# Kernel tuning notes

Measured on AMD Instinct MI355X. Metric: run time of the kernel, lower is better.

The kernel has to match this reference:

```python
import jax, jax.numpy as jnp
import numpy as np

B, L, D, H, E, K = 1, 512, 512, 512, 32, 2

def setup_inputs() -> dict:
    key = jax.random.key(0)
    ks = jax.random.split(key, 6)
    x = jax.random.normal(ks[0], (B, L, D), dtype=jnp.float32)
    router_scale = 1.0 + 0.02 * jax.random.normal(ks[1], (D,), dtype=jnp.float32)
    router_logits_w = 0.02 * jax.random.normal(ks[2], (D, E), dtype=jnp.float32)
    gating_einsum = 0.02 * jax.random.normal(ks[3], (E, 2, H, D), dtype=jnp.float32)
    linear_w = 0.02 * jax.random.normal(ks[4], (E, H, D), dtype=jnp.float32)
    per_expert_scale = 1.0 + 0.02 * jax.random.normal(ks[5], (E,), dtype=jnp.float32)
    return {"x": x, "router_scale": router_scale, "router_logits_w": router_logits_w,
            "gating_einsum": gating_einsum, "linear_w": linear_w,
            "per_expert_scale": per_expert_scale}

def reference(x, router_scale, router_logits_w, gating_einsum, linear_w, per_expert_scale):
    d = x.shape[-1]
    n_experts = router_logits_w.shape[-1]
    # RMSNorm without scale (fp32)
    x32 = x.astype(jnp.float32)
    var = jnp.mean(jnp.square(x32), axis=-1, keepdims=True)
    router_input = x32 * jax.lax.rsqrt(var + 1e-6)
    root_size = jax.lax.rsqrt(jnp.asarray(d, dtype=router_input.dtype))
    router_input = router_input * root_size * router_scale.astype(router_input.dtype)
    logits = jnp.dot(router_input, router_logits_w).astype(jnp.float32)  # [B,L,E]
    probs = jax.nn.softmax(logits, axis=-1)
    _, top_k_indices = jax.lax.top_k(logits, K)  # [B,L,K]
    indicator = jax.nn.one_hot(top_k_indices, n_experts, dtype=probs.dtype).sum(axis=-2)
    gate_weights = indicator * probs
    renorm = jnp.sum(gate_weights, axis=-1, keepdims=True)
    renorm = jnp.where(renorm > 0.0, renorm, 1.0)
    weights = probs / renorm
    top_k_weights = jnp.take_along_axis(weights, top_k_indices, axis=-1)  # [B,L,K]
    output = jnp.zeros_like(x)
    for ki in range(K):  # small fixed k; faithful to source's per-slot gather
        expert_idx = top_k_indices[:, :, ki]          # [B,L] int32
        expert_w = top_k_weights[:, :, ki]            # [B,L]
        gate_params = gating_einsum[expert_idx]       # [B,L,2,H,D] -- the big gather
        lin_params = linear_w[expert_idx]             # [B,L,H,D]
        escale = per_expert_scale[expert_idx]         # [B,L]
        gate_0 = jnp.einsum('bld,blhd->blh', x, gate_params[:, :, 0])
        gate_1 = jnp.einsum('bld,blhd->blh', x, gate_params[:, :, 1])
        activated = jax.nn.gelu(gate_0) * gate_1
        expert_out = jnp.einsum('blh,blhd->bld', activated, lin_params)
        output = output + expert_out * (escale * expert_w)[..., None]
    return output
```

## Files before the change

### kernel.cpp

```cpp
#include <hip/hip_runtime.h>
#include <hip/hip_bf16.h>
#include <math.h>

#define LTOK 512
#define DDIM 512
#define NEXP 32
#define HDIM 512

typedef __attribute__((ext_vector_type(8))) short short8;
typedef __attribute__((ext_vector_type(4))) float floatx4;

__device__ __forceinline__ unsigned bpack(float a, float b) {
    unsigned ua = __float_as_uint(a), ub = __float_as_uint(b);
    ua += 0x7FFFu + ((ua >> 16) & 1u);
    ub += 0x7FFFu + ((ub >> 16) & 1u);
    return (ua >> 16) | (ub & 0xFFFF0000u);
}


__global__ __launch_bounds__(64) void router_kernel(
    const float* __restrict__ x, const float* __restrict__ rs,
    const float* __restrict__ Wr, const float* __restrict__ pes,
    int* __restrict__ cnt, int* __restrict__ alist, float* __restrict__ slist,
    short* __restrict__ xb)
{
    const int t = blockIdx.x;
    const int lane = threadIdx.x;

    float xv[8];
    float ss = 0.f;
#pragma unroll
    for (int j = 0; j < 8; ++j) {
        xv[j] = x[t * DDIM + j * 64 + lane];
        ss += xv[j] * xv[j];
    }
#pragma unroll
    for (int j = 0; j < 8; ++j)
        xb[t * DDIM + j * 64 + lane] = (short)(bpack(xv[j], 0.f) & 0xFFFFu);

#pragma unroll
    for (int o = 32; o > 0; o >>= 1) ss += __shfl_xor(ss, o);
    const float var = ss * (1.0f / 512.0f);
    const float coef = rsqrtf(var + 1e-6f) * rsqrtf(512.0f);

    __shared__ float ri[DDIM];
#pragma unroll
    for (int j = 0; j < 8; ++j) {
        const int d = j * 64 + lane;
        ri[d] = xv[j] * coef * rs[d];
    }
    __syncthreads();

    const int e = lane & 31;
    const int half = lane >> 5;
    float lg = 0.f;
    const int dbeg = half * 256;
#pragma unroll 4
    for (int d = dbeg; d < dbeg + 256; ++d)
        lg = fmaf(ri[d], Wr[d * NEXP + e], lg);
    lg += __shfl_xor(lg, 32);

    __shared__ float lgs[NEXP];
    if (lane < 32) lgs[lane] = lg;
    __syncthreads();

    if (lane == 0) {
        int i0 = 0; float m0 = lgs[0];
        for (int i = 1; i < NEXP; ++i) if (lgs[i] > m0) { m0 = lgs[i]; i0 = i; }
        int i1 = -1; float m1 = -1e30f;
        for (int i = 0; i < NEXP; ++i) if (i != i0 && lgs[i] > m1) { m1 = lgs[i]; i1 = i; }
        const float e1 = expf(m1 - m0);
        const float inv = 1.0f / (1.0f + e1);
        const float w0 = inv, w1 = e1 * inv;

        int p0 = atomicAdd(&cnt[i0], 1);
        alist[i0 * LTOK + p0] = t * 2;
        slist[i0 * LTOK + p0] = w0 * pes[i0];
        int p1 = atomicAdd(&cnt[i1], 1);
        alist[i1 * LTOK + p1] = t * 2 + 1;
        slist[i1 * LTOK + p1] = w1 * pes[i1];
    }
}

__global__ __launch_bounds__(128, 1) void gates_kernel(
    const short* __restrict__ xb, const float* __restrict__ G,
    const int* __restrict__ cnt, const int* __restrict__ alist,
    short* __restrict__ act)
{
    const int e  = blockIdx.y;
    const int h0 = blockIdx.x * 16;
    const int Ne = cnt[e];
    if (Ne == 0) return;
    const int wv   = threadIdx.x >> 6;
    const int lane = threadIdx.x & 63;
    const int n    = lane & 15;
    const int quad = lane >> 4;

    __shared__ float xch[4][4][64];

    const float* Grow = G + ((size_t)((e * 2 + wv) * HDIM) + h0 + n) * DDIM;
    const int* al = alist + e * LTOK;

    for (int mb = 0; mb < Ne; mb += 64) {
        int arow[4];
#pragma unroll
        for (int i = 0; i < 4; ++i) {
            int s = mb + i * 16 + n;
            arow[i] = al[s < Ne ? s : Ne - 1] >> 1;
        }
        floatx4 acc[4] = {};

#pragma unroll 4
        for (int ks = 0; ks < 16; ++ks) {
            const int ko = ks * 32 + quad * 8;
            const floatx4 b0 = *(const floatx4*)(Grow + ko);
            const floatx4 b1 = *(const floatx4*)(Grow + ko + 4);
            union { short8 s; unsigned u[4]; } B;
            B.u[0] = bpack(b0.x, b0.y);
            B.u[1] = bpack(b0.z, b0.w);
            B.u[2] = bpack(b1.x, b1.y);
            B.u[3] = bpack(b1.z, b1.w);
#pragma unroll
            for (int i = 0; i < 4; ++i) {
                const short8 A = *(const short8*)(xb + (size_t)arow[i] * DDIM + ko);
                acc[i] = __builtin_amdgcn_mfma_f32_16x16x32_bf16(A, B.s, acc[i], 0, 0, 0);
            }
        }

        if (wv == 0) {
#pragma unroll
            for (int i = 0; i < 4; ++i)
#pragma unroll
                for (int r = 0; r < 4; ++r)
                    xch[i][r][lane] = acc[i][r];
        }
        __syncthreads();
        if (wv == 1) {
#pragma unroll
            for (int i = 0; i < 4; ++i) {
#pragma unroll
                for (int r = 0; r < 4; ++r) {
                    const int s = mb + i * 16 + quad * 4 + r;
                    if (s < Ne) {
                        const int a = al[s];
                        const float g0 = xch[i][r][lane];
                        const float g1 = acc[i][r];
                        const float u = 0.7978845608f * (g0 + 0.044715f * g0 * g0 * g0);
                        const float sg = 1.0f / (1.0f + __expf(-2.0f * u));
                        const float v = g0 * sg * g1;
                        act[(size_t)a * HDIM + h0 + n] = (short)(bpack(v, 0.f) & 0xFFFFu);
                    }
                }
            }
        }
        __syncthreads();
    }
}

__global__ __launch_bounds__(64, 1) void linear_kernel(
    const short* __restrict__ act, const float* __restrict__ Wl,
    const int* __restrict__ cnt, const int* __restrict__ alist,
    const float* __restrict__ slist, float* __restrict__ out)
{
    const int e  = blockIdx.y;
    const int d0 = blockIdx.x * 16;
    const int Ne = cnt[e];
    if (Ne == 0) return;
    const int lane = threadIdx.x;
    const int n    = lane & 15;
    const int quad = lane >> 4;

    const float* Wcol = Wl + (size_t)e * HDIM * DDIM + d0 + n;
    const int* al = alist + e * LTOK;
    const float* sl = slist + e * LTOK;

    for (int mb = 0; mb < Ne; mb += 64) {
        int arow[4];
#pragma unroll
        for (int i = 0; i < 4; ++i) {
            int s = mb + i * 16 + n;
            arow[i] = al[s < Ne ? s : Ne - 1];
        }
        floatx4 acc[4] = {};

#pragma unroll 2
        for (int ks = 0; ks < 16; ++ks) {
            const int ko = ks * 32 + quad * 8;
            float w[8];
#pragma unroll
            for (int j = 0; j < 8; ++j)
                w[j] = Wcol[(size_t)(ko + j) * DDIM];
            union { short8 s; unsigned u[4]; } B;
            B.u[0] = bpack(w[0], w[1]);
            B.u[1] = bpack(w[2], w[3]);
            B.u[2] = bpack(w[4], w[5]);
            B.u[3] = bpack(w[6], w[7]);
#pragma unroll
            for (int i = 0; i < 4; ++i) {
                const short8 A = *(const short8*)(act + (size_t)arow[i] * HDIM + ko);
                acc[i] = __builtin_amdgcn_mfma_f32_16x16x32_bf16(A, B.s, acc[i], 0, 0, 0);
            }
        }

#pragma unroll
        for (int i = 0; i < 4; ++i) {
#pragma unroll
            for (int r = 0; r < 4; ++r) {
                const int s = mb + i * 16 + quad * 4 + r;
                if (s < Ne) {
                    const int a = al[s];
                    atomicAdd(&out[(size_t)(a >> 1) * DDIM + d0 + n], acc[i][r] * sl[s]);
                }
            }
        }
    }
}

extern "C" void kernel_launch(void* const* d_in, const int* in_sizes, int n_in,
                              void* d_out, int out_size, void* d_ws, size_t ws_size,
                              hipStream_t stream)
{
    const float* x   = (const float*)d_in[0];
    const float* rs  = (const float*)d_in[1];
    const float* Wr  = (const float*)d_in[2];
    const float* G   = (const float*)d_in[3];
    const float* Wl  = (const float*)d_in[4];
    const float* pes = (const float*)d_in[5];
    float* out = (float*)d_out;

    char* ws = (char*)d_ws;
    int*   cnt   = (int*)(ws);
    int*   alist = (int*)(ws + 256);
    float* slist = (float*)(ws + 256 + 65536);
    short* xb    = (short*)(ws + 131328);
    short* act   = (short*)(ws + 655616);

    hipMemsetAsync(cnt, 0, NEXP * sizeof(int), stream);
    hipMemsetAsync(out, 0, (size_t)out_size * sizeof(float), stream);

    router_kernel<<<dim3(LTOK), dim3(64), 0, stream>>>(x, rs, Wr, pes, cnt, alist, slist, xb);
    gates_kernel<<<dim3(32, NEXP), dim3(128), 0, stream>>>(xb, G, cnt, alist, act);
    linear_kernel<<<dim3(32, NEXP), dim3(64), 0, stream>>>(act, Wl, cnt, alist, slist, out);
}
```

Baseline: 186.0 us.

## Split K dimension across waves in gates and linear kernels with LDS reduction

The gates kernel now uses four waves, each covering half the D reduction for one of the two gate projections. Partial sums are combined in shared memory before the GELU product. The linear kernel also uses four waves that each cover a quarter of H, reduced through shared memory before the atomic adds. The router dot product is split into four independent accumulators to shorten the FMA dependency chain. These changes aim to raise in-flight memory requests and latency hiding per block, at the cost of more shared memory traffic and extra barriers.

Result: faster. 165.4 us (-11.1%).

```diff
diff --git a/kernel.cpp b/kernel.cpp
--- a/kernel.cpp
+++ b/kernel.cpp
@@ -53,11 +53,16 @@
 
     const int e = lane & 31;
     const int half = lane >> 5;
-    float lg = 0.f;
     const int dbeg = half * 256;
+    float l0 = 0.f, l1 = 0.f, l2 = 0.f, l3 = 0.f;
 #pragma unroll 4
-    for (int d = dbeg; d < dbeg + 256; ++d)
-        lg = fmaf(ri[d], Wr[d * NEXP + e], lg);
+    for (int d = dbeg; d < dbeg + 256; d += 4) {
+        l0 = fmaf(ri[d + 0], Wr[(d + 0) * NEXP + e], l0);
+        l1 = fmaf(ri[d + 1], Wr[(d + 1) * NEXP + e], l1);
+        l2 = fmaf(ri[d + 2], Wr[(d + 2) * NEXP + e], l2);
+        l3 = fmaf(ri[d + 3], Wr[(d + 3) * NEXP + e], l3);
+    }
+    float lg = (l0 + l1) + (l2 + l3);
     lg += __shfl_xor(lg, 32);
 
     __shared__ float lgs[NEXP];
@@ -82,7 +87,7 @@
     }
 }
 
-__global__ __launch_bounds__(128, 1) void gates_kernel(
+__global__ __launch_bounds__(256, 4) void gates_kernel(
     const short* __restrict__ xb, const float* __restrict__ G,
     const int* __restrict__ cnt, const int* __restrict__ alist,
     short* __restrict__ act)
@@ -92,13 +97,16 @@
     const int Ne = cnt[e];
     if (Ne == 0) return;
     const int wv   = threadIdx.x >> 6;
+    const int g    = wv & 1;
+    const int kh   = wv >> 1;
     const int lane = threadIdx.x & 63;
     const int n    = lane & 15;
     const int quad = lane >> 4;
 
-    __shared__ float xch[4][4][64];
-
-    const float* Grow = G + ((size_t)((e * 2 + wv) * HDIM) + h0 + n) * DDIM;
+    __shared__ float red[4][4][4][64];
+
+    const float* Grow = G + ((size_t)((e * 2 + g) * HDIM) + h0 + n) * DDIM + kh * 256;
+    const short* xbh  = xb + kh * 256;
     const int* al = alist + e * LTOK;
 
     for (int mb = 0; mb < Ne; mb += 64) {
@@ -111,7 +119,7 @@
         floatx4 acc[4] = {};
 
 #pragma unroll 4
-        for (int ks = 0; ks < 16; ++ks) {
+        for (int ks = 0; ks < 8; ++ks) {
             const int ko = ks * 32 + quad * 8;
             const floatx4 b0 = *(const floatx4*)(Grow + ko);
             const floatx4 b1 = *(const floatx4*)(Grow + ko + 4);
@@ -122,34 +130,31 @@
             B.u[3] = bpack(b1.z, b1.w);
 #pragma unroll
             for (int i = 0; i < 4; ++i) {
-                const short8 A = *(const short8*)(xb + (size_t)arow[i] * DDIM + ko);
+                const short8 A = *(const short8*)(xbh + (size_t)arow[i] * DDIM + ko);
                 acc[i] = __builtin_amdgcn_mfma_f32_16x16x32_bf16(A, B.s, acc[i], 0, 0, 0);
             }
         }
 
-        if (wv == 0) {
-#pragma unroll
-            for (int i = 0; i < 4; ++i)
-#pragma unroll
-                for (int r = 0; r < 4; ++r)
-                    xch[i][r][lane] = acc[i][r];
-        }
-        __syncthreads();
-        if (wv == 1) {
-#pragma unroll
-            for (int i = 0; i < 4; ++i) {
-#pragma unroll
-                for (int r = 0; r < 4; ++r) {
-                    const int s = mb + i * 16 + quad * 4 + r;
-                    if (s < Ne) {
-                        const int a = al[s];
-                        const float g0 = xch[i][r][lane];
-                        const float g1 = acc[i][r];
-                        const float u = 0.7978845608f * (g0 + 0.044715f * g0 * g0 * g0);
-                        const float sg = 1.0f / (1.0f + __expf(-2.0f * u));
-                        const float v = g0 * sg * g1;
-                        act[(size_t)a * HDIM + h0 + n] = (short)(bpack(v, 0.f) & 0xFFFFu);
-                    }
+#pragma unroll
+        for (int i = 0; i < 4; ++i)
+#pragma unroll
+            for (int r = 0; r < 4; ++r)
+                red[wv][i][r][lane] = acc[i][r];
+        __syncthreads();
+
+        {
+            const int i = wv;
+#pragma unroll
+            for (int r = 0; r < 4; ++r) {
+                const int s = mb + i * 16 + quad * 4 + r;
+                if (s < Ne) {
+                    const int a = al[s];
+                    const float g0 = red[0][i][r][lane] + red[2][i][r][lane];
+                    const float g1 = red[1][i][r][lane] + red[3][i][r][lane];
+                    const float u = 0.7978845608f * (g0 + 0.044715f * g0 * g0 * g0);
+                    const float sg = 1.0f / (1.0f + __expf(-2.0f * u));
+                    const float v = g0 * sg * g1;
+                    act[(size_t)a * HDIM + h0 + n] = (short)(bpack(v, 0.f) & 0xFFFFu);
                 }
             }
         }
@@ -157,7 +162,7 @@
     }
 }
 
-__global__ __launch_bounds__(64, 1) void linear_kernel(
+__global__ __launch_bounds__(256, 4) void linear_kernel(
     const short* __restrict__ act, const float* __restrict__ Wl,
     const int* __restrict__ cnt, const int* __restrict__ alist,
     const float* __restrict__ slist, float* __restrict__ out)
@@ -166,9 +171,12 @@
     const int d0 = blockIdx.x * 16;
     const int Ne = cnt[e];
     if (Ne == 0) return;
-    const int lane = threadIdx.x;
+    const int wv   = threadIdx.x >> 6;
+    const int lane = threadIdx.x & 63;
     const int n    = lane & 15;
     const int quad = lane >> 4;
+
+    __shared__ float red[4][4][4][64];
 
     const float* Wcol = Wl + (size_t)e * HDIM * DDIM + d0 + n;
     const int* al = alist + e * LTOK;
@@ -184,8 +192,8 @@
         floatx4 acc[4] = {};
 
 #pragma unroll 2
-        for (int ks = 0; ks < 16; ++ks) {
-            const int ko = ks * 32 + quad * 8;
+        for (int ks = 0; ks < 4; ++ks) {
+            const int ko = wv * 128 + ks * 32 + quad * 8;
             float w[8];
 #pragma unroll
             for (int j = 0; j < 8; ++j)
@@ -203,16 +211,26 @@
         }
 
 #pragma unroll
-        for (int i = 0; i < 4; ++i) {
+        for (int i = 0; i < 4; ++i)
+#pragma unroll
+            for (int r = 0; r < 4; ++r)
+                red[wv][i][r][lane] = acc[i][r];
+        __syncthreads();
+
+        {
+            const int i = wv;
 #pragma unroll
             for (int r = 0; r < 4; ++r) {
                 const int s = mb + i * 16 + quad * 4 + r;
                 if (s < Ne) {
                     const int a = al[s];
-                    atomicAdd(&out[(size_t)(a >> 1) * DDIM + d0 + n], acc[i][r] * sl[s]);
+                    const float v = ((red[0][i][r][lane] + red[1][i][r][lane]) +
+                                     (red[2][i][r][lane] + red[3][i][r][lane])) * sl[s];
+                    atomicAdd(&out[(size_t)(a >> 1) * DDIM + d0 + n], v);
                 }
             }
         }
+        __syncthreads();
     }
 }
 
@@ -239,6 +257,6 @@
     hipMemsetAsync(out, 0, (size_t)out_size * sizeof(float), stream);
 
     router_kernel<<<dim3(LTOK), dim3(64), 0, stream>>>(x, rs, Wr, pes, cnt, alist, slist, xb);
-    gates_kernel<<<dim3(32, NEXP), dim3(128), 0, stream>>>(xb, G, cnt, alist, act);
-    linear_kernel<<<dim3(32, NEXP), dim3(64), 0, stream>>>(act, Wl, cnt, alist, slist, out);
-}
+    gates_kernel<<<dim3(32, NEXP), dim3(256), 0, stream>>>(xb, G, cnt, alist, act);
+    linear_kernel<<<dim3(32, NEXP), dim3(256), 0, stream>>>(act, Wl, cnt, alist, slist, out);
+}
```
